# Performance work log

Hardware: AMD Instinct MI355X
Metric: run time of the kernel (lower is better)

## Reference

```python
import jax, jax.numpy as jnp
import numpy as np

EPS = 1e-6

def _det3(m):
    return (m[..., 0, 0] * m[..., 1, 1] * m[..., 2, 2]
            + m[..., 0, 1] * m[..., 1, 2] * m[..., 2, 0]
            + m[..., 1, 0] * m[..., 2, 1] * m[..., 0, 2]
            - m[..., 2, 0] * m[..., 1, 1] * m[..., 0, 2]
            - m[..., 0, 0] * m[..., 2, 1] * m[..., 1, 2]
            - m[..., 1, 0] * m[..., 0, 1] * m[..., 2, 2])

def _inv3(m):
    a, b, c = m[..., 0, 0], m[..., 0, 1], m[..., 0, 2]
    d, e, f = m[..., 1, 0], m[..., 1, 1], m[..., 1, 2]
    g, h, i = m[..., 2, 0], m[..., 2, 1], m[..., 2, 2]
    adj = jnp.stack([
        jnp.stack([e * i - f * h, c * h - b * i, b * f - c * e], -1),
        jnp.stack([f * g - d * i, a * i - c * g, c * d - a * f], -1),
        jnp.stack([d * h - e * g, b * g - a * h, a * e - b * d], -1)], -2)
    return adj / _det3(m)[..., None, None]

def setup_inputs() -> dict:
    key = jax.random.key(0)
    ks = jax.random.split(key, 12)
    N, B, DH = 100000, 2048, 256
    idx = jnp.sort(jnp.concatenate([jnp.arange(B, dtype=jnp.int32),
                                    jax.random.randint(ks[0], (N - B,), 0, B, dtype=jnp.int32)]))
    return {
        "t": jax.random.uniform(ks[1], (B, 1), jnp.float32, 0.01, 0.99),
        "h": jax.random.normal(ks[2], (N, DH), jnp.float32),
        "pos": jax.random.normal(ks[3], (N, 3), jnp.float32),
        "eps_h": jax.random.normal(ks[4], (N, DH), jnp.float32),
        "eps_pos": jax.random.normal(ks[5], (N, 3), jnp.float32),
        "gparam_h": jax.random.normal(ks[6], (1, 1), jnp.float32),
        "gparam_pos": jax.random.normal(ks[7], (1, 1), jnp.float32),
        "W_mu": jax.random.normal(ks[8], (DH, DH), jnp.float32) / np.sqrt(DH),
        "W_r1": jax.random.normal(ks[9], (DH, 2 * DH), jnp.float32) / np.sqrt(DH),
        "W_r2": jax.random.normal(ks[10], (2 * DH, DH), jnp.float32) / np.sqrt(2 * DH),
        "index": idx,
        "num_graphs": B,
    }


def _forward(t, h, pos, eps_h, eps_pos, gparam_h, gparam_pos, W_mu, W_r1, W_r2, index, B):
    eye = jnp.eye(3, dtype=h.dtype)
    seg_sum = lambda x: jax.ops.segment_sum(x, index, num_segments=B)
    counts = seg_sum(jnp.ones((index.shape[0],), h.dtype))  # [B]

    def scatter_center(x):  # x - per-graph mean, gathered back
        mean = seg_sum(x) / counts[:, None]
        return x - mean[index]

    # volatility g(t): per-graph, gathered to nodes
    g_h = (0.1 + jax.nn.softplus(gparam_h) * t)[index]      # [N,1]
    g_pos = (0.1 + jax.nn.softplus(gparam_pos) * t)[index]  # [N,1]

    def f_net(t_, hh, pp):  # surrogate forward transformation f
        tn = t_[index]                                      # [N,1]
        mu_h = (hh @ W_mu) * (1.0 - tn)
        sigma_h = 0.1 + 0.9 * tn                            # [N,1]
        mu_pos = pp * (1.0 - tn)
        nrm = pp / (jnp.linalg.norm(pp, axis=-1, keepdims=True) + EPS)
        a = (0.2 + 0.8 * tn)[..., None]                     # [N,1,1]
        b = (0.1 * tn)[..., None]
        U = a * eye + b * (nrm[:, :, None] * nrm[:, None, :])  # [N,3,3]
        return mu_h, sigma_h, mu_pos, U

    def z_pos_fn(mu, U, eps):
        return mu + scatter_center(jnp.einsum('nij,nj->ni', U, eps))

    def score_pos_fn(eps, U, inv_U=None, C=None):
        if inv_U is None or C is None:
            inv_U = _inv3(U)
            inv_V = _inv3(seg_sum(inv_U))
            C = inv_V[index] @ (inv_U - eye)
        y = jnp.einsum('nji,nj->ni', inv_U, eps)
        ybar = seg_sum(y)
        c = jnp.einsum('nji,nj->ni', C, ybar[index])
        return scatter_center(c - y)  # zero_cog_score=True

    def solve_pos_fn(U, prel):
        inv_U = _inv3(U)
        inv_V = _inv3(seg_sum(inv_U))
        C = inv_V[index] @ (inv_U - eye)
        c = seg_sum(jnp.einsum('nij,nj->ni', C, prel))[index]
        eps = jnp.einsum('nij,nj->ni', inv_U, prel - c)
        return eps, inv_U, C

    bdrift = lambda dz, score, g: dz - 0.5 * g ** 2 * score

    # ---- target backward drift (time_derivative via jvp over t) ----
    (mu_h, sig_h, mu_p, U), (dmu_h, dsig_h, dmu_p, dU) = jax.jvp(
        lambda tt: f_net(tt, h, pos), (t,), (jnp.ones_like(t),))
    z_h = mu_h + sig_h * eps_h
    dz_h = dmu_h + dsig_h * eps_h
    z_p = z_pos_fn(mu_p, U, eps_pos)
    dz_p = z_pos_fn(dmu_p, dU, eps_pos)
    tgt_h = bdrift(dz_h, -eps_h / sig_h, g_h)
    tgt_p = bdrift(dz_p, score_pos_fn(eps_pos, U), g_pos)

    # ---- approximate backward drift ('x0' parameterization) ----
    h_r = jnp.tanh(z_h @ W_r1) @ W_r2   # reconstructor r
    pos_r = z_p * 0.9
    (mu_h2, sig_h2, mu_p2, U2), (dmu_h2, dsig_h2, dmu_p2, dU2) = jax.jvp(
        lambda tt: f_net(tt, h_r, pos_r), (t,), (jnp.ones_like(t),))
    eps_h2 = (z_h - mu_h2) / sig_h2
    eps_p2, inv_U2, C2 = solve_pos_fn(U2, z_p - mu_p2)
    dz_h2 = dmu_h2 + dsig_h2 * eps_h2
    dz_p2 = z_pos_fn(dmu_p2, dU2, eps_p2)
    apx_h = bdrift(dz_h2, -eps_h2 / sig_h2, g_h)
    apx_p = bdrift(dz_p2, score_pos_fn(eps_p2, U2, inv_U2, C2), g_pos)

    # ---- 'simple' loss: mse(approx/g, target/g) ----
    loss_h = jnp.mean(((apx_h - tgt_h) / g_h) ** 2)
    loss_p = jnp.mean(((apx_p - tgt_p) / g_pos) ** 2)
    return loss_h, loss_p


def reference(t, h, pos, eps_h, eps_pos, gparam_h, gparam_pos, W_mu, W_r1, W_r2, index, num_graphs):
    return _forward(t, h, pos, eps_h, eps_pos, gparam_h, gparam_pos, W_mu, W_r1, W_r2, index, num_graphs)
```

## Files before the change

kernel.cpp:

```cpp
#include <hip/hip_runtime.h>
#include <math.h>

#define NTHREADS 256
#define EPSC 1e-6f
#define NPL 3

typedef short bf16x8 __attribute__((ext_vector_type(8)));
typedef float f32x4  __attribute__((ext_vector_type(4)));

#define GLDS(srcp, dstp) __builtin_amdgcn_global_load_lds( \
    (const __attribute__((address_space(1))) void*)(srcp), \
    (__attribute__((address_space(3))) void*)(dstp), 16, 0, 0)

__device__ __forceinline__ ushort f2bf(float x) {
  union { float f; unsigned u; } v; v.f = x;
  unsigned r = v.u + 0x7FFFu + ((v.u >> 16) & 1u);
  return (ushort)(r >> 16);
}
__device__ __forceinline__ float bf2f(ushort x) {
  union { unsigned u; float f; } v; v.u = ((unsigned)x) << 16;
  return v.f;
}
__device__ __forceinline__ bf16x8 pack8(float4 a, float4 b) {
  bf16x8 r;
  r[0]=(short)f2bf(a.x); r[1]=(short)f2bf(a.y); r[2]=(short)f2bf(a.z); r[3]=(short)f2bf(a.w);
  r[4]=(short)f2bf(b.x); r[5]=(short)f2bf(b.y); r[6]=(short)f2bf(b.z); r[7]=(short)f2bf(b.w);
  return r;
}
__device__ __forceinline__ float tanh_fast(float x) {
  float xc = fminf(fmaxf(x, -15.f), 15.f);
  float e = __expf(2.f * xc);
  return (e - 1.f) / (e + 1.f);
}

__device__ __forceinline__ void inv3x3(const float m[9], float o[9]) {
  float a=m[0],b=m[1],c=m[2],d=m[3],e=m[4],f=m[5],g=m[6],h=m[7],i=m[8];
  float det = a*e*i + b*f*g + d*h*c - g*e*c - a*h*f - d*b*i;
  float r = 1.0f/det;
  o[0]=(e*i-f*h)*r; o[1]=(c*h-b*i)*r; o[2]=(b*f-c*e)*r;
  o[3]=(f*g-d*i)*r; o[4]=(a*i-c*g)*r; o[5]=(c*d-a*f)*r;
  o[6]=(d*h-e*g)*r; o[7]=(b*g-a*h)*r; o[8]=(a*e-b*d)*r;
}

__device__ __forceinline__ float wred(float v) {
#pragma unroll
  for (int o = 32; o > 0; o >>= 1) v += __shfl_xor(v, o, 64);
  return v;
}

__global__ __launch_bounds__(64) void pos_branch_v4b(
    int N, const float* __restrict__ pos, const float* __restrict__ epsp,
    const int* __restrict__ index, const float* __restrict__ t,
    const float* __restrict__ gpp, double* __restrict__ lossp)
{
  const int b = blockIdx.x;
  const int lane = threadIdx.x;

  int lo = 0, hi = N;
  while (lo < hi) { int mid = (lo + hi) >> 1; if (index[mid] < b) lo = mid + 1; else hi = mid; }
  const int start = lo;
  hi = N;
  while (lo < hi) { int mid = (lo + hi) >> 1; if (index[mid] < b + 1) lo = mid + 1; else hi = mid; }
  const int end = lo;
  const int cnt = end - start;
  const float fn = (float)cnt, rc = 1.0f / fn;

  const float tn  = t[b];
  const float a1  = 0.2f + 0.8f*tn, b1 = 0.1f*tn;
  const float omt = 1.0f - tn;
  const float sp  = log1pf(expf(gpp[0]));
  const float gp  = 0.1f + sp*tn;
  const float hg  = 0.5f*gp*gp;
  const float rgp = 1.0f/gp;
  const float pscale = 1.0f - 0.9f*omt;

  float iU[NPL][9], yv[NPL][3], wv[NPL][3], dwv[NPL][3], pv[NPL][3];
  float Vs[9] = {0}, wb[3] = {0}, dwb[3] = {0}, yb[3] = {0};
#pragma unroll
  for (int k = 0; k < NPL; ++k) {
    const int n = start + k*64 + lane;
    if (n < end) {
      const float px = pos[3*(size_t)n+0], py = pos[3*(size_t)n+1], pz = pos[3*(size_t)n+2];
      const float ex = epsp[3*(size_t)n+0], ey = epsp[3*(size_t)n+1], ez = epsp[3*(size_t)n+2];
      pv[k][0]=px; pv[k][1]=py; pv[k][2]=pz;
      const float pn = sqrtf(px*px+py*py+pz*pz) + EPSC;
      const float nx = px/pn, ny = py/pn, nz = pz/pn;
      const float nd = nx*ex + ny*ey + nz*ez;
      wv[k][0]=a1*ex + b1*nd*nx; wv[k][1]=a1*ey + b1*nd*ny; wv[k][2]=a1*ez + b1*nd*nz;
      dwv[k][0]=0.8f*ex + 0.1f*nd*nx; dwv[k][1]=0.8f*ey + 0.1f*nd*ny; dwv[k][2]=0.8f*ez + 0.1f*nd*nz;
      const float U[9] = { a1 + b1*nx*nx, b1*nx*ny,      b1*nx*nz,
                           b1*ny*nx,      a1 + b1*ny*ny, b1*ny*nz,
                           b1*nz*nx,      b1*nz*ny,      a1 + b1*nz*nz };
      inv3x3(U, iU[k]);
      yv[k][0] = iU[k][0]*ex + iU[k][3]*ey + iU[k][6]*ez;
      yv[k][1] = iU[k][1]*ex + iU[k][4]*ey + iU[k][7]*ez;
      yv[k][2] = iU[k][2]*ex + iU[k][5]*ey + iU[k][8]*ez;
#pragma unroll
      for (int j = 0; j < 9; ++j) Vs[j] += iU[k][j];
#pragma unroll
      for (int j = 0; j < 3; ++j) { wb[j]+=wv[k][j]; dwb[j]+=dwv[k][j]; yb[j]+=yv[k][j]; }
    }
  }
#pragma unroll
  for (int j = 0; j < 9; ++j) Vs[j] = wred(Vs[j]);
#pragma unroll
  for (int j = 0; j < 3; ++j) { wb[j]=wred(wb[j]); dwb[j]=wred(dwb[j]); yb[j]=wred(yb[j]); }

  float iV[9]; inv3x3(Vs, iV);
  float wm[3], dwm[3], u1[3], s1m[3];
#pragma unroll
  for (int i = 0; i < 3; ++i) { wm[i] = wb[i]*rc; dwm[i] = dwb[i]*rc; }
#pragma unroll
  for (int i = 0; i < 3; ++i) u1[i] = iV[0*3+i]*yb[0] + iV[1*3+i]*yb[1] + iV[2*3+i]*yb[2];
#pragma unroll
  for (int i = 0; i < 3; ++i) {
    const float csy = Vs[0*3+i]*u1[0] + Vs[1*3+i]*u1[1] + Vs[2*3+i]*u1[2] - fn*u1[i];
    s1m[i] = (csy - yb[i]) * rc;
  }

  float tg[NPL][3], zp[NPL][3], iU2[NPL][9], qv[NPL][3];
  float Vs2[9] = {0}, qs[3] = {0}, ps[3] = {0};
#pragma unroll
  for (int k = 0; k < NPL; ++k) {
    const int n = start + k*64 + lane;
    if (n < end) {
#pragma unroll
      for (int i = 0; i < 3; ++i) {
        const float c1 = iU[k][0*3+i]*u1[0] + iU[k][1*3+i]*u1[1] + iU[k][2*3+i]*u1[2] - u1[i];
        const float score1 = c1 - yv[k][i] - s1m[i];
        tg[k][i] = -pv[k][i] + dwv[k][i] - dwm[i] - hg*score1;
        zp[k][i] = pv[k][i]*omt + wv[k][i] - wm[i];
      }
      const float rx = 0.9f*zp[k][0], ry = 0.9f*zp[k][1], rz = 0.9f*zp[k][2];
      const float rn = sqrtf(rx*rx+ry*ry+rz*rz) + EPSC;
      const float nx = rx/rn, ny = ry/rn, nz = rz/rn;
      const float U2[9] = { a1 + b1*nx*nx, b1*nx*ny,      b1*nx*nz,
                            b1*ny*nx,      a1 + b1*ny*ny, b1*ny*nz,
                            b1*nz*nx,      b1*nz*ny,      a1 + b1*nz*nz };
      inv3x3(U2, iU2[k]);
      float prel[3];
#pragma unroll
      for (int i = 0; i < 3; ++i) prel[i] = zp[k][i]*pscale;
#pragma unroll
      for (int i = 0; i < 3; ++i)
        qv[k][i] = iU2[k][i*3+0]*prel[0] + iU2[k][i*3+1]*prel[1] + iU2[k][i*3+2]*prel[2];
#pragma unroll
      for (int j = 0; j < 9; ++j) Vs2[j] += iU2[k][j];
#pragma unroll
      for (int j = 0; j < 3; ++j) { qs[j] += qv[k][j]; ps[j] += prel[j]; }
    }
  }
#pragma unroll
  for (int j = 0; j < 9; ++j) Vs2[j] = wred(Vs2[j]);
#pragma unroll
  for (int j = 0; j < 3; ++j) { qs[j] = wred(qs[j]); ps[j] = wred(ps[j]); }

  float iV2[9]; inv3x3(Vs2, iV2);
  float cb2[3];
#pragma unroll
  for (int i = 0; i < 3; ++i)
    cb2[i] = iV2[i*3+0]*(qs[0]-ps[0]) + iV2[i*3+1]*(qs[1]-ps[1]) + iV2[i*3+2]*(qs[2]-ps[2]);

  float y2v[NPL][3], dw2v[NPL][3];
  float yb2[3] = {0}, dwb2[3] = {0};
#pragma unroll
  for (int k = 0; k < NPL; ++k) {
    const int n = start + k*64 + lane;
    if (n < end) {
      float e[3];
#pragma unroll
      for (int i = 0; i < 3; ++i)
        e[i] = qv[k][i] - (iU2[k][i*3+0]*cb2[0] + iU2[k][i*3+1]*cb2[1] + iU2[k][i*3+2]*cb2[2]);
#pragma unroll
      for (int i = 0; i < 3; ++i)
        y2v[k][i] = iU2[k][0*3+i]*e[0] + iU2[k][1*3+i]*e[1] + iU2[k][2*3+i]*e[2];
      const float rx = 0.9f*zp[k][0], ry = 0.9f*zp[k][1], rz = 0.9f*zp[k][2];
      const float rn = sqrtf(rx*rx+ry*ry+rz*rz) + EPSC;
      const float nx = rx/rn, ny = ry/rn, nz = rz/rn;
      const float nd = nx*e[0] + ny*e[1] + nz*e[2];
      dw2v[k][0] = 0.8f*e[0] + 0.1f*nd*nx;
      dw2v[k][1] = 0.8f*e[1] + 0.1f*nd*ny;
      dw2v[k][2] = 0.8f*e[2] + 0.1f*nd*nz;
#pragma unroll
      for (int j = 0; j < 3; ++j) { yb2[j] += y2v[k][j]; dwb2[j] += dw2v[k][j]; }
    }
  }
#pragma unroll
  for (int j = 0; j < 3; ++j) { yb2[j] = wred(yb2[j]); dwb2[j] = wred(dwb2[j]); }

  float u2[3], s2m[3], dw2m[3];
#pragma unroll
  for (int i = 0; i < 3; ++i) u2[i] = iV2[0*3+i]*yb2[0] + iV2[1*3+i]*yb2[1] + iV2[2*3+i]*yb2[2];
#pragma unroll
  for (int i = 0; i < 3; ++i) {
    const float csy = Vs2[0*3+i]*u2[0] + Vs2[1*3+i]*u2[1] + Vs2[2*3+i]*u2[2] - fn*u2[i];
    s2m[i] = (csy - yb2[i]) * rc;
    dw2m[i] = dwb2[i] * rc;
  }

  float acc = 0.0f;
#pragma unroll
  for (int k = 0; k < NPL; ++k) {
    const int n = start + k*64 + lane;
    if (n < end) {
#pragma unroll
      for (int i = 0; i < 3; ++i) {
        const float c2 = iU2[k][0*3+i]*u2[0] + iU2[k][1*3+i]*u2[1] + iU2[k][2*3+i]*u2[2] - u2[i];
        const float score2 = c2 - y2v[k][i] - s2m[i];
        const float dz2 = -0.9f*zp[k][i] + dw2v[k][i] - dw2m[i];
        const float apx = dz2 - hg*score2;
        const float d = (apx - tg[k][i]) * rgp;
        acc += d*d;
      }
    }
  }
  acc = wred(acc);
  if (lane == 0) atomicAdd(lossp, (double)acc);
}

__global__ __launch_bounds__(NTHREADS) void prep_weights_v4b(
    const float4* __restrict__ wr2, ushort4* __restrict__ wr2b, int n4w,
    const float* __restrict__ wmu, ushort* __restrict__ wmut,
    const float* __restrict__ wr1, ushort* __restrict__ wr1t)
{
  __shared__ float ts[32][33];
  const int bid = blockIdx.x;
  if (bid < 128) {
    const int i = bid*NTHREADS + threadIdx.x;
    if (i < n4w) {
      float4 v = wr2[i];
      wr2b[i] = make_ushort4(f2bf(v.x), f2bf(v.y), f2bf(v.z), f2bf(v.w));
    }
  } else if (bid < 192) {
    const int vb = bid - 128;
    const int nb = (vb & 7)*32, kb = (vb >> 3)*32;
    const int tx = threadIdx.x & 31, ty = threadIdx.x >> 5;
#pragma unroll
    for (int r = 0; r < 4; ++r)
      ts[ty + r*8][tx] = wmu[(size_t)(kb + ty + r*8)*256 + nb + tx];
    __syncthreads();
#pragma unroll
    for (int r = 0; r < 4; ++r)
      wmut[(size_t)(nb + ty + r*8)*256 + kb + tx] = f2bf(ts[tx][ty + r*8]);
  } else {
    const int vb = bid - 192;
    const int nb = (vb & 15)*32, kb = (vb >> 4)*32;
    const int tx = threadIdx.x & 31, ty = threadIdx.x >> 5;
#pragma unroll
    for (int r = 0; r < 4; ++r)
      ts[ty + r*8][tx] = wr1[(size_t)(kb + ty + r*8)*512 + nb + tx];
    __syncthreads();
#pragma unroll
    for (int r = 0; r < 4; ++r)
      wr1t[(size_t)(nb + ty + r*8)*256 + kb + tx] = f2bf(ts[tx][ty + r*8]);
  }
}

__global__ __launch_bounds__(256) void wcomb_gemm_v4b(
    const ushort* __restrict__ A, const ushort* __restrict__ Bt,
    int K, int Nn, int Mvalid, ushort* __restrict__ OutB)
{
  __shared__ __align__(16) ushort As[128*32];
  __shared__ __align__(16) ushort Bs[128*32];
  const int tid = threadIdx.x;
  const int row0 = blockIdx.y*128, col0 = blockIdx.x*128;
  const int wave = tid >> 6, lane = tid & 63;
  const int wm = (wave & 1)*64, wn = (wave >> 1)*64;
  const int lm = lane & 15, lq = lane >> 4;

  f32x4 acc[4][4];
#pragma unroll
  for (int i = 0; i < 4; ++i)
#pragma unroll
    for (int j = 0; j < 4; ++j) { acc[i][j][0]=0.f; acc[i][j][1]=0.f; acc[i][j][2]=0.f; acc[i][j][3]=0.f; }

  const int c0 = tid, c1 = tid + 256;
  const int r0a = c0 >> 2, k0a = (c0 & 3) << 3;
  const int r1a = c1 >> 2, k1a = (c1 & 3) << 3;

  for (int k0 = 0; k0 < K; k0 += 32) {
    __syncthreads();
    GLDS(A  + (size_t)(row0 + r0a)*K + k0 + k0a, As + c0*8);
    GLDS(A  + (size_t)(row0 + r1a)*K + k0 + k1a, As + c1*8);
    GLDS(Bt + (size_t)(col0 + r0a)*K + k0 + k0a, Bs + c0*8);
    GLDS(Bt + (size_t)(col0 + r1a)*K + k0 + k1a, Bs + c1*8);
    __syncthreads();

    bf16x8 af[4], bfr[4];
#pragma unroll
    for (int i = 0; i < 4; ++i)
      af[i] = *(const bf16x8*)&As[(wm + i*16 + lm)*32 + lq*8];
#pragma unroll
    for (int j = 0; j < 4; ++j)
      bfr[j] = *(const bf16x8*)&Bs[(wn + j*16 + lm)*32 + lq*8];
#pragma unroll
    for (int i = 0; i < 4; ++i)
#pragma unroll
      for (int j = 0; j < 4; ++j)
        acc[i][j] = __builtin_amdgcn_mfma_f32_16x16x32_bf16(af[i], bfr[j], acc[i][j], 0, 0, 0);
  }

#pragma unroll
  for (int i = 0; i < 4; ++i) {
#pragma unroll
    for (int reg = 0; reg < 4; ++reg) {
      const int r = row0 + wm + i*16 + lq*4 + reg;
#pragma unroll
      for (int j = 0; j < 4; ++j) {
        const int cc = col0 + wn + j*16 + lm;
        OutB[(size_t)cc*Mvalid + r] = f2bf(-acc[i][j][reg]);
      }
    }
  }
}

__global__ __launch_bounds__(256, 2) void h_branch_v4b(
    const float* __restrict__ hf, const ushort* __restrict__ wmut,
    const ushort* __restrict__ wr1t, const ushort* __restrict__ wct,
    const float* __restrict__ eps, const int* __restrict__ index,
    const float* __restrict__ t, const float* __restrict__ gph,
    int N, double* __restrict__ lossAcc)
{
  __shared__ __align__(16) ushort zs[64*256];
  __shared__ __align__(16) ushort t1s[64*128];

  const int wave = threadIdx.x >> 6, lane = threadIdx.x & 63;
  const int row0 = blockIdx.x * 64;
  const int lm = lane & 15, lq = lane >> 4;
  const int wn  = wave * 64;
  const int wn2 = wave * 32;

  f32x4 acc[4][4];
#pragma unroll
  for (int i = 0; i < 4; ++i)
#pragma unroll
    for (int j = 0; j < 4; ++j) { acc[i][j][0]=0.f; acc[i][j][1]=0.f; acc[i][j][2]=0.f; acc[i][j][3]=0.f; }

#pragma unroll
  for (int k = 0; k < 8; ++k) {
    bf16x8 a_[4], b_[4];
#pragma unroll
    for (int i = 0; i < 4; ++i) {
      int r = row0 + i*16 + lm; if (r >= N) r = N - 1;
      const float4* p = (const float4*)(hf + (size_t)r*256 + k*32 + lq*8);
      a_[i] = pack8(p[0], p[1]);
    }
#pragma unroll
    for (int j = 0; j < 4; ++j)
      b_[j] = *(const bf16x8*)(wmut + (size_t)(wn + j*16 + lm)*256 + k*32 + lq*8);
#pragma unroll
    for (int i = 0; i < 4; ++i)
#pragma unroll
      for (int j = 0; j < 4; ++j)
        acc[i][j] = __builtin_amdgcn_mfma_f32_16x16x32_bf16(a_[i], b_[j], acc[i][j], 0, 0, 0);
  }

#pragma unroll
  for (int i = 0; i < 4; ++i) {
#pragma unroll
    for (int reg = 0; reg < 4; ++reg) {
      const int rb = i*16 + lq*4 + reg;
      const int r = row0 + rb;
      const int rcl = (r < N) ? r : (N - 1);
      const float tn = t[index[rcl]];
      const float s0 = 1.0f - tn, s1 = 0.1f + 0.9f*tn;
#pragma unroll
      for (int j = 0; j < 4; ++j) {
        const int cc = wn + j*16 + lm;
        const float z = acc[i][j][reg]*s0 + s1*eps[(size_t)rcl*256 + cc];
        zs[rb*256 + (cc ^ ((rb & 7) << 3))] = f2bf(z);
      }
    }
  }
  __syncthreads();

  for (int c2 = 0; c2 < 4; ++c2) {
    f32x4 acct[4][2];
#pragma unroll
    for (int i = 0; i < 4; ++i)
#pragma unroll
      for (int j = 0; j < 2; ++j) { acct[i][j][0]=0.f; acct[i][j][1]=0.f; acct[i][j][2]=0.f; acct[i][j][3]=0.f; }

#pragma unroll
    for (int k = 0; k < 8; ++k) {
      bf16x8 az[4], b_[2];
#pragma unroll
      for (int i = 0; i < 4; ++i) {
        const int r = i*16 + lm;
        const int c = k*32 + lq*8;
        az[i] = *(const bf16x8*)&zs[r*256 + (c ^ ((r & 7) << 3))];
      }
#pragma unroll
      for (int j = 0; j < 2; ++j)
        b_[j] = *(const bf16x8*)(wr1t + (size_t)(c2*128 + wn2 + j*16 + lm)*256 + k*32 + lq*8);
#pragma unroll
      for (int i = 0; i < 4; ++i)
#pragma unroll
        for (int j = 0; j < 2; ++j)
          acct[i][j] = __builtin_amdgcn_mfma_f32_16x16x32_bf16(az[i], b_[j], acct[i][j], 0, 0, 0);
    }

    __syncthreads();
#pragma unroll
    for (int i = 0; i < 4; ++i)
#pragma unroll
      for (int j = 0; j < 2; ++j)
#pragma unroll
        for (int reg = 0; reg < 4; ++reg) {
          const int rb = i*16 + lq*4 + reg;
          const int c = wn2 + j*16 + lm;
          t1s[rb*128 + (c ^ ((rb & 7) << 3))] = f2bf(tanh_fast(acct[i][j][reg]));
        }
    __syncthreads();

#pragma unroll
    for (int k = 0; k < 4; ++k) {
      bf16x8 at[4], b_[4];
#pragma unroll
      for (int i = 0; i < 4; ++i) {
        const int r = i*16 + lm;
        const int c = k*32 + lq*8;
        at[i] = *(const bf16x8*)&t1s[r*128 + (c ^ ((r & 7) << 3))];
      }
#pragma unroll
      for (int j = 0; j < 4; ++j)
        b_[j] = *(const bf16x8*)(wct + (size_t)(wn + j*16 + lm)*512 + c2*128 + k*32 + lq*8);
#pragma unroll
      for (int i = 0; i < 4; ++i)
#pragma unroll
        for (int j = 0; j < 4; ++j)
          acc[i][j] = __builtin_amdgcn_mfma_f32_16x16x32_bf16(at[i], b_[j], acc[i][j], 0, 0, 0);
    }
  }

  const float sp = log1pf(expf(gph[0]));
  float local = 0.f;
#pragma unroll
  for (int i = 0; i < 4; ++i) {
#pragma unroll
    for (int reg = 0; reg < 4; ++reg) {
      const int r = row0 + i*16 + lq*4 + reg;
      if (r < N) {
        const float tn = t[index[r]];
        const float gh  = 0.1f + sp*tn;
        const float sig = 0.1f + 0.9f*tn;
        const float fac = 1.0f + (0.9f + 0.5f*gh*gh/sig)*(1.0f - tn)/sig;
        const float sc  = fac/gh;
#pragma unroll
        for (int j = 0; j < 4; ++j) {
          const float d = acc[i][j][reg] * sc;
          local += d*d;
        }
      }
    }
  }
  double dv = (double)local;
#pragma unroll
  for (int off = 32; off > 0; off >>= 1) dv += __shfl_down(dv, off, 64);
  if (lane == 0) atomicAdd(lossAcc, dv);
}

__global__ void finalize_v4b(const double* lossh, const double* lossp,
                             float* out, int N, int DH)
{
  if (threadIdx.x == 0) {
    out[0] = (float)(lossh[0] / ((double)N * (double)DH));
    out[1] = (float)(lossp[0] / ((double)N * 3.0));
  }
}

extern "C" void kernel_launch(void* const* d_in, const int* in_sizes, int n_in,
                              void* d_out, int out_size, void* d_ws, size_t ws_size,
                              hipStream_t stream) {
  const float* t      = (const float*)d_in[0];
  const float* h      = (const float*)d_in[1];
  const float* pos    = (const float*)d_in[2];
  const float* eps_h  = (const float*)d_in[3];
  const float* eps_p  = (const float*)d_in[4];
  const float* gph    = (const float*)d_in[5];
  const float* gpp    = (const float*)d_in[6];
  const float* W_mu   = (const float*)d_in[7];
  const float* W_r1   = (const float*)d_in[8];
  const float* W_r2   = (const float*)d_in[9];
  const int*   index  = (const int*)d_in[10];
  const int B = in_sizes[0];
  const int N = in_sizes[10];
  const int DH = 256, DH2 = 512;

  char* ws = (char*)d_ws;
  size_t off = 0;
  auto alloc = [&](size_t nbytes) { size_t o = off; off += (nbytes + 255) & ~(size_t)255; return o; };

  size_t o_loss = alloc(16);
  size_t o_wmut = alloc((size_t)DH*DH*2);
  size_t o_wr1t = alloc((size_t)DH2*DH*2);
  size_t o_wr2b = alloc((size_t)DH2*DH*2);
  size_t o_wct  = alloc((size_t)DH*DH2*2);

  hipMemsetAsync(ws + o_loss, 0, 16, stream);

  double* lossh = (double*)(ws + o_loss);
  double* lossp = lossh + 1;
  ushort* wmut = (ushort*)(ws + o_wmut);
  ushort* wr1t = (ushort*)(ws + o_wr1t);
  ushort* wr2b = (ushort*)(ws + o_wr2b);
  ushort* wct  = (ushort*)(ws + o_wct);

  pos_branch_v4b<<<B, 64, 0, stream>>>(N, pos, eps_p, index, t, gpp, lossp);

  prep_weights_v4b<<<320, NTHREADS, 0, stream>>>(
      (const float4*)W_r2, (ushort4*)wr2b, DH2*DH/4,
      W_mu, wmut, W_r1, wr1t);

  wcomb_gemm_v4b<<<dim3(DH/128, DH2/128), 256, 0, stream>>>(
      wr2b, wmut, DH, DH, DH2, wct);

  const int HB = (N + 63) / 64;
  h_branch_v4b<<<HB, 256, 0, stream>>>(
      h, wmut, wr1t, wct, eps_h, index, t, gph, N, lossh);

  finalize_v4b<<<1, 64, 0, stream>>>(lossh, lossp, (float*)d_out, N, DH);
}
```

Baseline: 489.2 us.

## Double-buffer weight tiles into LDS and prefetch activations in h branch

The h-branch kernel now stages its weight tiles (W_mu, W_r1, combined W) per wave into LDS through async global_load_lds with double buffering and explicit vmcnt waits, and it prefetches the next K-slice of h into registers. The goal is to overlap global memory latency with MFMA work instead of loading B fragments straight from global memory. Per-row time scalars are also precomputed in the prep kernel so the h kernel skips index/t gathers and transcendentals, and the per-wave atomics are merged into one per block. In exchange the kernel uses 32KB more LDS, which may reduce occupancy, and it adds fragile hand-written waitcnt counts.

```diff
diff --git a/kernel.cpp b/kernel.cpp
--- a/kernel.cpp
+++ b/kernel.cpp
@@ -48,7 +48,7 @@
   return v;
 }
 
-__global__ __launch_bounds__(64) void pos_branch_v4b(
+__global__ __launch_bounds__(64) void pos_branch_v5(
     int N, const float* __restrict__ pos, const float* __restrict__ epsp,
     const int* __restrict__ index, const float* __restrict__ t,
     const float* __restrict__ gpp, double* __restrict__ lossp)
@@ -218,10 +218,13 @@
   if (lane == 0) atomicAdd(lossp, (double)acc);
 }
 
-__global__ __launch_bounds__(NTHREADS) void prep_weights_v4b(
+__global__ __launch_bounds__(NTHREADS) void prep_v5(
     const float4* __restrict__ wr2, ushort4* __restrict__ wr2b, int n4w,
     const float* __restrict__ wmu, ushort* __restrict__ wmut,
-    const float* __restrict__ wr1, ushort* __restrict__ wr1t)
+    const float* __restrict__ wr1, ushort* __restrict__ wr1t,
+    const float* __restrict__ t, const int* __restrict__ index,
+    const float* __restrict__ gph,
+    float2* __restrict__ zsc, float* __restrict__ lsc, int Nn)
 {
   __shared__ float ts[32][33];
   const int bid = blockIdx.x;
@@ -242,7 +245,7 @@
 #pragma unroll
     for (int r = 0; r < 4; ++r)
       wmut[(size_t)(nb + ty + r*8)*256 + kb + tx] = f2bf(ts[tx][ty + r*8]);
-  } else {
+  } else if (bid < 320) {
     const int vb = bid - 192;
     const int nb = (vb & 15)*32, kb = (vb >> 4)*32;
     const int tx = threadIdx.x & 31, ty = threadIdx.x >> 5;
@@ -253,10 +256,21 @@
 #pragma unroll
     for (int r = 0; r < 4; ++r)
       wr1t[(size_t)(nb + ty + r*8)*256 + kb + tx] = f2bf(ts[tx][ty + r*8]);
-  }
-}
-
-__global__ __launch_bounds__(256) void wcomb_gemm_v4b(
+  } else {
+    const int r = (bid - 320)*NTHREADS + threadIdx.x;
+    if (r < Nn) {
+      const float tn = t[index[r]];
+      zsc[r] = make_float2(1.0f - tn, 0.1f + 0.9f*tn);
+      const float sp  = log1pf(expf(gph[0]));
+      const float gh  = 0.1f + sp*tn;
+      const float sig = 0.1f + 0.9f*tn;
+      const float fac = 1.0f + (0.9f + 0.5f*gh*gh/sig)*(1.0f - tn)/sig;
+      lsc[r] = fac/gh;
+    }
+  }
+}
+
+__global__ __launch_bounds__(256) void wcomb_gemm_v5(
     const ushort* __restrict__ A, const ushort* __restrict__ Bt,
     int K, int Nn, int Mvalid, ushort* __restrict__ OutB)
 {
@@ -314,21 +328,43 @@
   }
 }
 
-__global__ __launch_bounds__(256, 2) void h_branch_v4b(
+__global__ __launch_bounds__(256, 2) void h_branch_v5(
     const float* __restrict__ hf, const ushort* __restrict__ wmut,
     const ushort* __restrict__ wr1t, const ushort* __restrict__ wct,
-    const float* __restrict__ eps, const int* __restrict__ index,
-    const float* __restrict__ t, const float* __restrict__ gph,
+    const float* __restrict__ eps, const float2* __restrict__ zsc,
+    const float* __restrict__ lsc,
     int N, double* __restrict__ lossAcc)
 {
   __shared__ __align__(16) ushort zs[64*256];
   __shared__ __align__(16) ushort t1s[64*128];
+  __shared__ __align__(16) ushort bstg[4*4096];
+  __shared__ double redsm[4];
 
   const int wave = threadIdx.x >> 6, lane = threadIdx.x & 63;
   const int row0 = blockIdx.x * 64;
   const int lm = lane & 15, lq = lane >> 4;
   const int wn  = wave * 64;
   const int wn2 = wave * 32;
+  ushort* const bsw = bstg + wave*4096;
+
+  int arow[4];
+#pragma unroll
+  for (int i = 0; i < 4; ++i) {
+    int r = row0 + i*16 + lm; if (r >= N) r = N - 1;
+    arow[i] = r;
+  }
+
+  float4 aCur[8], aNxt[8];
+#pragma unroll
+  for (int i = 0; i < 4; ++i) {
+    const float4* p = (const float4*)(hf + (size_t)arow[i]*256 + lq*8);
+    aCur[2*i] = p[0]; aCur[2*i+1] = p[1];
+  }
+#pragma unroll
+  for (int c = 0; c < 4; ++c) {
+    const int ch = c*64 + lane;
+    GLDS(wmut + (size_t)(wn + (ch>>2))*256 + ((ch&3)<<3), bsw + ch*8);
+  }
 
   f32x4 acc[4][4];
 #pragma unroll
@@ -338,21 +374,47 @@
 
 #pragma unroll
   for (int k = 0; k < 8; ++k) {
+    if (k < 7) {
+#pragma unroll
+      for (int i = 0; i < 4; ++i) {
+        const float4* p = (const float4*)(hf + (size_t)arow[i]*256 + (k+1)*32 + lq*8);
+        aNxt[2*i] = p[0]; aNxt[2*i+1] = p[1];
+      }
+#pragma unroll
+      for (int c = 0; c < 4; ++c) {
+        const int ch = c*64 + lane;
+        GLDS(wmut + (size_t)(wn + (ch>>2))*256 + (k+1)*32 + ((ch&3)<<3),
+             bsw + ((k+1)&1)*2048 + ch*8);
+      }
+      asm volatile("s_waitcnt vmcnt(12)" ::: "memory");
+    } else {
+      asm volatile("s_waitcnt vmcnt(0)" ::: "memory");
+    }
+    __builtin_amdgcn_sched_barrier(0);
+
+    const ushort* cb = bsw + (k&1)*2048;
     bf16x8 a_[4], b_[4];
 #pragma unroll
-    for (int i = 0; i < 4; ++i) {
-      int r = row0 + i*16 + lm; if (r >= N) r = N - 1;
-      const float4* p = (const float4*)(hf + (size_t)r*256 + k*32 + lq*8);
-      a_[i] = pack8(p[0], p[1]);
-    }
+    for (int i = 0; i < 4; ++i) a_[i] = pack8(aCur[2*i], aCur[2*i+1]);
 #pragma unroll
     for (int j = 0; j < 4; ++j)
-      b_[j] = *(const bf16x8*)(wmut + (size_t)(wn + j*16 + lm)*256 + k*32 + lq*8);
+      b_[j] = *(const bf16x8*)&cb[(j*16 + lm)*32 + lq*8];
 #pragma unroll
     for (int i = 0; i < 4; ++i)
 #pragma unroll
       for (int j = 0; j < 4; ++j)
         acc[i][j] = __builtin_amdgcn_mfma_f32_16x16x32_bf16(a_[i], b_[j], acc[i][j], 0, 0, 0);
+
+    if (k < 7) {
+#pragma unroll
+      for (int q = 0; q < 8; ++q) aCur[q] = aNxt[q];
+    }
+  }
+
+#pragma unroll
+  for (int c = 0; c < 2; ++c) {
+    const int ch = c*64 + lane;
+    GLDS(wr1t + (size_t)(wn2 + (ch>>2))*256 + ((ch&3)<<3), bsw + ch*8);
   }
 
 #pragma unroll
@@ -362,12 +424,11 @@
       const int rb = i*16 + lq*4 + reg;
       const int r = row0 + rb;
       const int rcl = (r < N) ? r : (N - 1);
-      const float tn = t[index[rcl]];
-      const float s0 = 1.0f - tn, s1 = 0.1f + 0.9f*tn;
+      const float2 sz = zsc[rcl];
 #pragma unroll
       for (int j = 0; j < 4; ++j) {
         const int cc = wn + j*16 + lm;
-        const float z = acc[i][j][reg]*s0 + s1*eps[(size_t)rcl*256 + cc];
+        const float z = acc[i][j][reg]*sz.x + sz.y*eps[(size_t)rcl*256 + cc];
         zs[rb*256 + (cc ^ ((rb & 7) << 3))] = f2bf(z);
       }
     }
@@ -383,6 +444,20 @@
 
 #pragma unroll
     for (int k = 0; k < 8; ++k) {
+      if (k < 7) {
+#pragma unroll
+        for (int c = 0; c < 2; ++c) {
+          const int ch = c*64 + lane;
+          GLDS(wr1t + (size_t)(c2*128 + wn2 + (ch>>2))*256 + (k+1)*32 + ((ch&3)<<3),
+               bsw + ((k+1)&1)*2048 + ch*8);
+        }
+        asm volatile("s_waitcnt vmcnt(2)" ::: "memory");
+      } else {
+        asm volatile("s_waitcnt vmcnt(0)" ::: "memory");
+      }
+      __builtin_amdgcn_sched_barrier(0);
+
+      const ushort* cb = bsw + (k&1)*2048;
       bf16x8 az[4], b_[2];
 #pragma unroll
       for (int i = 0; i < 4; ++i) {
@@ -392,7 +467,7 @@
       }
 #pragma unroll
       for (int j = 0; j < 2; ++j)
-        b_[j] = *(const bf16x8*)(wr1t + (size_t)(c2*128 + wn2 + j*16 + lm)*256 + k*32 + lq*8);
+        b_[j] = *(const bf16x8*)&cb[(j*16 + lm)*32 + lq*8];
 #pragma unroll
       for (int i = 0; i < 4; ++i)
 #pragma unroll
@@ -400,7 +475,13 @@
           acct[i][j] = __builtin_amdgcn_mfma_f32_16x16x32_bf16(az[i], b_[j], acct[i][j], 0, 0, 0);
     }
 
+#pragma unroll
+    for (int c = 0; c < 4; ++c) {
+      const int ch = c*64 + lane;
+      GLDS(wct + (size_t)(wn + (ch>>2))*512 + c2*128 + ((ch&3)<<3), bsw + ch*8);
+    }
     __syncthreads();
+
 #pragma unroll
     for (int i = 0; i < 4; ++i)
 #pragma unroll
@@ -415,6 +496,20 @@
 
 #pragma unroll
     for (int k = 0; k < 4; ++k) {
+      if (k < 3) {
+#pragma unroll
+        for (int c = 0; c < 4; ++c) {
+          const int ch = c*64 + lane;
+          GLDS(wct + (size_t)(wn + (ch>>2))*512 + c2*128 + (k+1)*32 + ((ch&3)<<3),
+               bsw + ((k+1)&1)*2048 + ch*8);
+        }
+        asm volatile("s_waitcnt vmcnt(4)" ::: "memory");
+      } else {
+        asm volatile("s_waitcnt vmcnt(0)" ::: "memory");
+      }
+      __builtin_amdgcn_sched_barrier(0);
+
+      const ushort* cb = bsw + (k&1)*2048;
       bf16x8 at[4], b_[4];
 #pragma unroll
       for (int i = 0; i < 4; ++i) {
@@ -424,16 +519,23 @@
       }
 #pragma unroll
       for (int j = 0; j < 4; ++j)
-        b_[j] = *(const bf16x8*)(wct + (size_t)(wn + j*16 + lm)*512 + c2*128 + k*32 + lq*8);
+        b_[j] = *(const bf16x8*)&cb[(j*16 + lm)*32 + lq*8];
 #pragma unroll
       for (int i = 0; i < 4; ++i)
 #pragma unroll
         for (int j = 0; j < 4; ++j)
           acc[i][j] = __builtin_amdgcn_mfma_f32_16x16x32_bf16(at[i], b_[j], acc[i][j], 0, 0, 0);
     }
-  }
-
-  const float sp = log1pf(expf(gph[0]));
+
+    if (c2 < 3) {
+#pragma unroll
+      for (int c = 0; c < 2; ++c) {
+        const int ch = c*64 + lane;
+        GLDS(wr1t + (size_t)((c2+1)*128 + wn2 + (ch>>2))*256 + ((ch&3)<<3), bsw + ch*8);
+      }
+    }
+  }
+
   float local = 0.f;
 #pragma unroll
   for (int i = 0; i < 4; ++i) {
@@ -441,11 +543,7 @@
     for (int reg = 0; reg < 4; ++reg) {
       const int r = row0 + i*16 + lq*4 + reg;
       if (r < N) {
-        const float tn = t[index[r]];
-        const float gh  = 0.1f + sp*tn;
-        const float sig = 0.1f + 0.9f*tn;
-        const float fac = 1.0f + (0.9f + 0.5f*gh*gh/sig)*(1.0f - tn)/sig;
-        const float sc  = fac/gh;
+        const float sc = lsc[r];
 #pragma unroll
         for (int j = 0; j < 4; ++j) {
           const float d = acc[i][j][reg] * sc;
@@ -457,11 +555,14 @@
   double dv = (double)local;
 #pragma unroll
   for (int off = 32; off > 0; off >>= 1) dv += __shfl_down(dv, off, 64);
-  if (lane == 0) atomicAdd(lossAcc, dv);
-}
-
-__global__ void finalize_v4b(const double* lossh, const double* lossp,
-                             float* out, int N, int DH)
+  if (lane == 0) redsm[wave] = dv;
+  __syncthreads();
+  if (threadIdx.x == 0)
+    atomicAdd(lossAcc, redsm[0] + redsm[1] + redsm[2] + redsm[3]);
+}
+
+__global__ void finalize_v5(const double* lossh, const double* lossp,
+                            float* out, int N, int DH)
 {
   if (threadIdx.x == 0) {
     out[0] = (float)(lossh[0] / ((double)N * (double)DH));
@@ -496,6 +597,8 @@
   size_t o_wr1t = alloc((size_t)DH2*DH*2);
   size_t o_wr2b = alloc((size_t)DH2*DH*2);
   size_t o_wct  = alloc((size_t)DH*DH2*2);
+  size_t o_zsc  = alloc((size_t)N*8);
+  size_t o_lsc  = alloc((size_t)N*4);
 
   hipMemsetAsync(ws + o_loss, 0, 16, stream);
 
@@ -505,19 +608,23 @@
   ushort* wr1t = (ushort*)(ws + o_wr1t);
   ushort* wr2b = (ushort*)(ws + o_wr2b);
   ushort* wct  = (ushort*)(ws + o_wct);
-
-  pos_branch_v4b<<<B, 64, 0, stream>>>(N, pos, eps_p, index, t, gpp, lossp);
-
-  prep_weights_v4b<<<320, NTHREADS, 0, stream>>>(
+  float2* zsc  = (float2*)(ws + o_zsc);
+  float*  lsc  = (float*)(ws + o_lsc);
+
+  pos_branch_v5<<<B, 64, 0, stream>>>(N, pos, eps_p, index, t, gpp, lossp);
+
+  const int scB = (N + NTHREADS - 1) / NTHREADS;
+  prep_v5<<<320 + scB, NTHREADS, 0, stream>>>(
       (const float4*)W_r2, (ushort4*)wr2b, DH2*DH/4,
-      W_mu, wmut, W_r1, wr1t);
-
-  wcomb_gemm_v4b<<<dim3(DH/128, DH2/128), 256, 0, stream>>>(
+      W_mu, wmut, W_r1, wr1t,
+      t, index, gph, zsc, lsc, N);
+
+  wcomb_gemm_v5<<<dim3(DH/128, DH2/128), 256, 0, stream>>>(
       wr2b, wmut, DH, DH, DH2, wct);
 
   const int HB = (N + 63) / 64;
-  h_branch_v4b<<<HB, 256, 0, stream>>>(
-      h, wmut, wr1t, wct, eps_h, index, t, gph, N, lossh);
-
-  finalize_v4b<<<1, 64, 0, stream>>>(lossh, lossp, (float*)d_out, N, DH);
-}
+  h_branch_v5<<<HB, 256, 0, stream>>>(
+      h, wmut, wr1t, wct, eps_h, zsc, lsc, N, lossh);
+
+  finalize_v5<<<1, 64, 0, stream>>>(lossh, lossp, (float*)d_out, N, DH);
+}
```

Result: slower. 501.3 us (+2.5%).
